# Performance work log

Measured on AMD Instinct MI355X. Metric: run time of the kernel, lower is better.

## Reference

```python
import jax, jax.numpy as jnp
import numpy as np

DIM = 1024
N_HEADS = 16
HEAD_DIM = 64
SEQ = 2048
BATCH = 2


def setup_inputs() -> dict:
    key = jax.random.key(0)
    ks = jax.random.split(key, 7)
    scale = 1.0 / np.sqrt(DIM)
    return {
        "q": jax.random.normal(ks[0], (BATCH, SEQ, DIM), dtype=jnp.float32),
        "k": jax.random.normal(ks[1], (BATCH, SEQ, DIM), dtype=jnp.float32),
        "v": jax.random.normal(ks[2], (BATCH, SEQ, DIM), dtype=jnp.float32),
        "wq": jax.random.normal(ks[3], (DIM, DIM), dtype=jnp.float32) * scale,
        "wk": jax.random.normal(ks[4], (DIM, DIM), dtype=jnp.float32) * scale,
        "wv": jax.random.normal(ks[5], (DIM, DIM), dtype=jnp.float32) * scale,
        "wo": jax.random.normal(ks[6], (DIM, DIM), dtype=jnp.float32) * scale,
    }


def reference(q, k, v, wq, wk, wv, wo):
    B, S, D = q.shape
    # Linear layers: y = x @ W.T (torch nn.Linear convention)
    qh = (q @ wq.T).reshape(B, S, N_HEADS, HEAD_DIM).transpose(0, 2, 1, 3)  # [B,H,S,hd]
    kh = (k @ wk.T).reshape(B, S, N_HEADS, HEAD_DIM).transpose(0, 2, 1, 3)
    vh = (v @ wv.T).reshape(B, S, N_HEADS, HEAD_DIM).transpose(0, 2, 1, 3)
    score = jnp.einsum('bhqd,bhkd->bhqk', qh, kh) / jnp.sqrt(jnp.float32(HEAD_DIM))
    # causal mask: upper triangle (j > i) set to -inf
    causal = jnp.tril(jnp.ones((S, S), dtype=bool))
    score = jnp.where(causal[None, None], score, -jnp.inf)
    attn = jax.nn.softmax(score, axis=-1)
    out = jnp.einsum('bhqk,bhkd->bhqd', attn, vh)  # [B,H,S,hd]
    out = out.transpose(0, 2, 1, 3).reshape(B, S, D)
    return out @ wo.T
```

## Files before the change

kernel.cpp:

```cpp
#include <hip/hip_runtime.h>

typedef unsigned short u16;
typedef unsigned int   u32;
typedef __bf16 bf16x8 __attribute__((ext_vector_type(8)));
typedef float  f32x4  __attribute__((ext_vector_type(4)));
typedef unsigned short u16x4 __attribute__((ext_vector_type(4)));
typedef unsigned short u16x8 __attribute__((ext_vector_type(8)));
typedef unsigned int   u32x2 __attribute__((ext_vector_type(2)));
typedef unsigned int   u32x4 __attribute__((ext_vector_type(4)));

#define DIM   1024
#define SEQ   2048
#define NH    16
#define HD    64
#define NBATCH 2

#define NEG_INF (-__builtin_inff())
#define QSCALE 0.1803368801111204f


__device__ __forceinline__ u16 f2bf(float f) {
  unsigned u = __float_as_uint(f);
  unsigned r = (u + 0x7FFFu + ((u >> 16) & 1u)) >> 16;
  return (u16)r;
}

__device__ __forceinline__ u32 pkbf(float a, float b) {
#if __has_builtin(__builtin_amdgcn_cvt_pk_bf16_f32)
  typedef __bf16 bf16x2 __attribute__((ext_vector_type(2)));
  bf16x2 t = __builtin_amdgcn_cvt_pk_bf16_f32(a, b);
  return __builtin_bit_cast(u32, t);
#else
  return (u32)f2bf(a) | ((u32)f2bf(b) << 16);
#endif
}

__device__ __forceinline__ void gload16(const void* g, void* lds_uniform) {
  __builtin_amdgcn_global_load_lds(
      (__attribute__((address_space(1))) void*)(size_t)g,
      (__attribute__((address_space(3))) void*)lds_uniform,
      16, 0, 0);
}


__global__ __launch_bounds__(256) void cvt_all(
    const float* __restrict__ q, const float* __restrict__ k, const float* __restrict__ v,
    const float* __restrict__ wq, const float* __restrict__ wk, const float* __restrict__ wv,
    const float* __restrict__ wo, u16* __restrict__ ws) {
  const size_t M = 1u << 20;
  int b = blockIdx.x;
  const float* src;
  u16* dst;
  int idx;
  if (b < 6144) {
    int t = b >> 11; idx = b & 2047;
    src = (t == 0) ? q : (t == 1) ? k : v;
    dst = ws + (size_t)t * 4 * M;
  } else {
    int t = (b - 6144) >> 9; idx = (b - 6144) & 511;
    src = (t == 0) ? wq : (t == 1) ? wk : (t == 2) ? wv : wo;
    dst = ws + (12 + (size_t)t) * M;
  }
  size_t i = ((size_t)idx * 256 + threadIdx.x) * 8;
  float4 a = *(const float4*)(src + i);
  float4 c = *(const float4*)(src + i + 4);
  u16x8 o;
  o[0] = f2bf(a.x); o[1] = f2bf(a.y); o[2] = f2bf(a.z); o[3] = f2bf(a.w);
  o[4] = f2bf(c.x); o[5] = f2bf(c.y); o[6] = f2bf(c.z); o[7] = f2bf(c.w);
  *(u16x8*)(dst + i) = o;
}


__device__ __forceinline__ void gemm128_core(const u16* __restrict__ A,
                                             const u16* __restrict__ W,
                                             int bm, int bn,
                                             u16* lds, f32x4 (&acc)[4][4]) {
  const int K = 1024;
  const int tid = threadIdx.x;
  const int wave = tid >> 6, lane = tid & 63;
  const int quad = lane >> 4, l15 = lane & 15;
  const int warp_m = wave >> 1, warp_n = wave & 1;

  const int c0 = wave * 128 + lane, c1 = c0 + 64;
  const u16* Ag0 = A + (size_t)(bm * 128 + (c0 >> 2)) * K + (c0 & 3) * 8;
  const u16* Ag1 = A + (size_t)(bm * 128 + (c1 >> 2)) * K + (c1 & 3) * 8;
  const u16* Wg0 = W + (size_t)(bn * 128 + (c0 >> 2)) * K + (c0 & 3) * 8;
  const u16* Wg1 = W + (size_t)(bn * 128 + (c1 >> 2)) * K + (c1 & 3) * 8;
  const int lA0 = (wave * 2 + 0) * 512;
  const int lA1 = (wave * 2 + 1) * 512;
  const int lB0 = 4096 + (wave * 2 + 0) * 512;
  const int lB1 = 4096 + (wave * 2 + 1) * 512;

  gload16(Ag0, lds + lA0);
  gload16(Ag1, lds + lA1);
  gload16(Wg0, lds + lB0);
  gload16(Wg1, lds + lB1);

  for (int k0 = 0; k0 < K; k0 += 32) {
    const int buf = (k0 >> 5) & 1;
    u16* cur = lds + buf * 8192;
    __syncthreads();
    if (k0 + 32 < K) {
      u16* nxt = lds + (buf ^ 1) * 8192;
      gload16(Ag0 + k0 + 32, nxt + lA0);
      gload16(Ag1 + k0 + 32, nxt + lA1);
      gload16(Wg0 + k0 + 32, nxt + lB0);
      gload16(Wg1 + k0 + 32, nxt + lB1);
    }

    bf16x8 af[4], bfr[4];
#pragma unroll
    for (int i = 0; i < 4; ++i) {
      af[i]  = *(const bf16x8*)(cur + (warp_m * 64 + i * 16 + l15) * 32 + quad * 8);
      bfr[i] = *(const bf16x8*)(cur + 4096 + (warp_n * 64 + i * 16 + l15) * 32 + quad * 8);
    }
#pragma unroll
    for (int i = 0; i < 4; ++i)
#pragma unroll
      for (int j = 0; j < 4; ++j)
        acc[i][j] = __builtin_amdgcn_mfma_f32_16x16x32_bf16(af[i], bfr[j], acc[i][j], 0, 0, 0);
  }
}

__global__ __launch_bounds__(256) void gemm_qkv(
    const u16* __restrict__ qb, const u16* __restrict__ kb, const u16* __restrict__ vb,
    const u16* __restrict__ wq, const u16* __restrict__ wk, const u16* __restrict__ wv,
    u16* __restrict__ Qo, u16* __restrict__ Ko, u16* __restrict__ Vt) {
  __shared__ __align__(16) u16 lds[2][8192];
  const int id = blockIdx.x;
  const int c = id & 7, bn = (id >> 3) & 7, t = id >> 6;
  const int g = c + 8 * t;
  const int bm = g & 31, z = g >> 5;

  const u16* A = (z == 0) ? qb : (z == 1) ? kb : vb;
  const u16* W = (z == 0) ? wq : (z == 1) ? wk : wv;
  f32x4 acc[4][4] = {};
  gemm128_core(A, W, bm, bn, &lds[0][0], acc);

  const int tid = threadIdx.x;
  const int wave = tid >> 6, lane = tid & 63;
  const int quad = lane >> 4, l15 = lane & 15;
  const int warp_m = wave >> 1, warp_n = wave & 1;
#pragma unroll
  for (int i = 0; i < 4; ++i)
#pragma unroll
    for (int j = 0; j < 4; ++j) {
      int s0 = bm * 128 + warp_m * 64 + i * 16 + quad * 4;
      int n  = bn * 128 + warp_n * 64 + j * 16 + l15;
      int bb = s0 >> 11, sl0 = s0 & 2047, h = n >> 6, d = n & 63;
      if (z == 2) {
        int pos = (sl0 & ~63) | (sl0 & 32) | ((sl0 & 12) << 1) | ((sl0 & 16) >> 2);
        int psw = (pos & ~63) | ((((pos >> 3) & 7) ^ (d & 7)) << 3) | (pos & 7);
        u16x4 pv;
        pv[0] = f2bf(acc[i][j][0]); pv[1] = f2bf(acc[i][j][1]);
        pv[2] = f2bf(acc[i][j][2]); pv[3] = f2bf(acc[i][j][3]);
        *(u16x4*)(Vt + ((size_t)(bb * NH + h) * HD + d) * SEQ + psw) = pv;
      } else if (z == 1) {
#pragma unroll
        for (int r = 0; r < 4; ++r) {
          int s = sl0 + r;
          int dsw = (((d >> 3) ^ (s & 7)) << 3) | (d & 7);
          Ko[((size_t)(bb * NH + h) * SEQ + s) * HD + dsw] = f2bf(acc[i][j][r]);
        }
      } else {
#pragma unroll
        for (int r = 0; r < 4; ++r)
          Qo[((size_t)(bb * NH + h) * SEQ + sl0 + r) * HD + d] = f2bf(acc[i][j][r] * QSCALE);
      }
    }
}

__global__ __launch_bounds__(256) void gemm_out(
    const u16* __restrict__ A, const u16* __restrict__ W, float* __restrict__ Out) {
  __shared__ __align__(16) u16 lds[2][8192];
  const int id = blockIdx.x;
  const int bn = (id >> 3) & 7;
  const int bm = (id & 7) + 8 * (id >> 6);
  f32x4 acc[4][4] = {};
  gemm128_core(A, W, bm, bn, &lds[0][0], acc);

  const int tid = threadIdx.x;
  const int wave = tid >> 6, lane = tid & 63;
  const int quad = lane >> 4, l15 = lane & 15;
  const int warp_m = wave >> 1, warp_n = wave & 1;
#pragma unroll
  for (int i = 0; i < 4; ++i)
#pragma unroll
    for (int j = 0; j < 4; ++j)
#pragma unroll
      for (int r = 0; r < 4; ++r) {
        int m = bm * 128 + warp_m * 64 + i * 16 + quad * 4 + r;
        int n = bn * 128 + warp_n * 64 + j * 16 + l15;
        Out[(size_t)m * DIM + n] = acc[i][j][r];
      }
}


__global__ __launch_bounds__(256) void attn_kernel(
    const u16* __restrict__ Q, const u16* __restrict__ K,
    const u16* __restrict__ Vt, u16* __restrict__ O) {
  __shared__ __align__(16) u16 Kl[2][4096];
  __shared__ __align__(16) u16 Vl[2][4096];

  const int tid = threadIdx.x;
  const int wave = tid >> 6, lane = tid & 63;
  const int quad = lane >> 4, l15 = lane & 15;
  const int bx = blockIdx.x;
  const int bh = bx & 31;
  const int qt = 31 - (bx >> 5);
  const int b = bh >> 4, h = bh & 15;

  const u16* qbase = Q + ((size_t)bh * SEQ + qt * 64 + wave * 16 + l15) * HD + quad * 8;
  const bf16x8 qf0 = *(const bf16x8*)(qbase);
  const bf16x8 qf1 = *(const bf16x8*)(qbase + 32);

  bf16x8 ones;
#pragma unroll
  for (int i = 0; i < 8; ++i) ones[i] = (__bf16)1.0f;

  f32x4 o[4] = {};
  f32x4 o4 = {};
  float m_run = NEG_INF;

  const int c0 = wave * 128 + lane, c1 = c0 + 64;
  const u16* Ksrc = K + (size_t)bh * SEQ * HD;
  const u16* Vsrc = Vt + (size_t)bh * HD * SEQ;
  const int sw0 = ((quad ^ (l15 & 7)) << 3);
  const int sw1 = (((4 + quad) ^ (l15 & 7)) << 3);

  {
    gload16(Ksrc + (size_t)c0 * 8, &Kl[0][(wave * 2 + 0) * 512]);
    gload16(Ksrc + (size_t)c1 * 8, &Kl[0][(wave * 2 + 1) * 512]);
    gload16(Vsrc + (size_t)(c0 >> 3) * SEQ + (c0 & 7) * 8, &Vl[0][(wave * 2 + 0) * 512]);
    gload16(Vsrc + (size_t)(c1 >> 3) * SEQ + (c1 & 7) * 8, &Vl[0][(wave * 2 + 1) * 512]);
  }

  for (int kt = 0; kt <= qt; ++kt) {
    const int buf = kt & 1;
    __syncthreads();
    if (kt < qt) {
      const int nb = buf ^ 1;
      const size_t kb = (size_t)(kt + 1) * 64;
      gload16(Ksrc + (kb * HD) + (size_t)c0 * 8, &Kl[nb][(wave * 2 + 0) * 512]);
      gload16(Ksrc + (kb * HD) + (size_t)c1 * 8, &Kl[nb][(wave * 2 + 1) * 512]);
      gload16(Vsrc + (size_t)(c0 >> 3) * SEQ + kb + (c0 & 7) * 8, &Vl[nb][(wave * 2 + 0) * 512]);
      gload16(Vsrc + (size_t)(c1 >> 3) * SEQ + kb + (c1 & 7) * 8, &Vl[nb][(wave * 2 + 1) * 512]);
    }

    f32x4 s[4];
#pragma unroll
    for (int kn = 0; kn < 4; ++kn) {
      const u16* arow = &Kl[buf][(kn * 16 + l15) * 64];
      bf16x8 kf0 = *(const bf16x8*)(arow + sw0);
      bf16x8 kf1 = *(const bf16x8*)(arow + sw1);
      f32x4 z = {};
      z = __builtin_amdgcn_mfma_f32_16x16x32_bf16(kf0, qf0, z, 0, 0, 0);
      z = __builtin_amdgcn_mfma_f32_16x16x32_bf16(kf1, qf1, z, 0, 0, 0);
      s[kn] = z;
    }

    if (kt == qt) {
      const int qloc = wave * 16 + l15;
#pragma unroll
      for (int kn = 0; kn < 4; ++kn)
#pragma unroll
        for (int r = 0; r < 4; ++r)
          if (kn * 16 + quad * 4 + r > qloc) s[kn][r] = NEG_INF;
    }

    float mr = NEG_INF;
#pragma unroll
    for (int kn = 0; kn < 4; ++kn)
#pragma unroll
      for (int r = 0; r < 4; ++r) mr = fmaxf(mr, s[kn][r]);
    mr = fmaxf(mr, __shfl_xor(mr, 16));
    mr = fmaxf(mr, __shfl_xor(mr, 32));
    const float mnew = fmaxf(m_run, mr);
    const float alpha = __builtin_amdgcn_exp2f(m_run - mnew);
    m_run = mnew;
#pragma unroll
    for (int kn = 0; kn < 4; ++kn)
#pragma unroll
      for (int r = 0; r < 4; ++r)
        s[kn][r] = __builtin_amdgcn_exp2f(s[kn][r] - mnew);

    u32x4 t0, t1;
    t0[0] = pkbf(s[0][0], s[0][1]); t0[1] = pkbf(s[0][2], s[0][3]);
    t0[2] = pkbf(s[1][0], s[1][1]); t0[3] = pkbf(s[1][2], s[1][3]);
    t1[0] = pkbf(s[2][0], s[2][1]); t1[1] = pkbf(s[2][2], s[2][3]);
    t1[2] = pkbf(s[3][0], s[3][1]); t1[3] = pkbf(s[3][2], s[3][3]);
    bf16x8 pf0 = __builtin_bit_cast(bf16x8, t0);
    bf16x8 pf1 = __builtin_bit_cast(bf16x8, t1);

#pragma unroll
    for (int n = 0; n < 4; ++n)
#pragma unroll
      for (int r = 0; r < 4; ++r) o[n][r] *= alpha;
#pragma unroll
    for (int r = 0; r < 4; ++r) o4[r] *= alpha;

    o4 = __builtin_amdgcn_mfma_f32_16x16x32_bf16(ones, pf0, o4, 0, 0, 0);
    o4 = __builtin_amdgcn_mfma_f32_16x16x32_bf16(ones, pf1, o4, 0, 0, 0);

#pragma unroll
    for (int n = 0; n < 4; ++n) {
      const u16* vrow = &Vl[buf][(n * 16 + l15) * 64];
      bf16x8 vf0 = *(const bf16x8*)(vrow + sw0);
      bf16x8 vf1 = *(const bf16x8*)(vrow + sw1);
      o[n] = __builtin_amdgcn_mfma_f32_16x16x32_bf16(vf0, pf0, o[n], 0, 0, 0);
      o[n] = __builtin_amdgcn_mfma_f32_16x16x32_bf16(vf1, pf1, o[n], 0, 0, 0);
    }
  }

  const float inv = 1.f / o4[0];
  const int srow = qt * 64 + wave * 16 + l15;
  u16* obase = O + ((size_t)b * SEQ + srow) * DIM + h * HD + quad * 4;
#pragma unroll
  for (int n = 0; n < 4; ++n) {
    u32x2 st;
    st[0] = pkbf(o[n][0] * inv, o[n][1] * inv);
    st[1] = pkbf(o[n][2] * inv, o[n][3] * inv);
    *(u32x2*)(obase + n * 16) = st;
  }
}


extern "C" void kernel_launch(void* const* d_in, const int* in_sizes, int n_in,
                              void* d_out, int out_size, void* d_ws, size_t ws_size,
                              hipStream_t stream) {
  (void)in_sizes; (void)n_in; (void)out_size; (void)ws_size;
  const float* q  = (const float*)d_in[0];
  const float* k  = (const float*)d_in[1];
  const float* v  = (const float*)d_in[2];
  const float* wq = (const float*)d_in[3];
  const float* wk = (const float*)d_in[4];
  const float* wv = (const float*)d_in[5];
  const float* wo = (const float*)d_in[6];

  u16* ws = (u16*)d_ws;
  const size_t EL = 1u << 20;
  u16* QB = ws + 0 * EL;
  u16* KB = ws + 4 * EL;
  u16* VB = ws + 8 * EL;
  u16* WQ = ws + 12 * EL;
  u16* WK = ws + 13 * EL;
  u16* WV = ws + 14 * EL;
  u16* WO = ws + 15 * EL;
  u16* Qw = ws + 16 * EL;
  u16* Kw = ws + 20 * EL;
  u16* Vtw = ws + 24 * EL;
  u16* AO = ws + 28 * EL;

  cvt_all<<<8192, 256, 0, stream>>>(q, k, v, wq, wk, wv, wo, ws);
  gemm_qkv<<<768, 256, 0, stream>>>(QB, KB, VB, WQ, WK, WV, Qw, Kw, Vtw);
  attn_kernel<<<1024, 256, 0, stream>>>(Qw, Kw, Vtw, AO);
  gemm_out<<<256, 256, 0, stream>>>(AO, WO, (float*)d_out);
}
```

Measured before the change: 200.6 us.

## Shrink GEMM tiles to 128x64, swizzle LDS, reorder attention query tiles

Both GEMM kernels switch from 128x128 to 128x64 output tiles, which doubles the grid sizes (768 to 1536 and 256 to 512) to give better occupancy on the many-CU device. The change adds a launch-bounds occupancy hint of 6 blocks for gemm_qkv. It also adds an XOR swizzle on the LDS layout of the K-chunks to cut bank conflicts. The attention kernel's query-tile order becomes a serpentine pattern to balance causal work across waves of blocks. Smaller tiles reduce data reuse per block and add more A-matrix reloads.

```diff
diff --git a/kernel.cpp b/kernel.cpp
--- a/kernel.cpp
+++ b/kernel.cpp
@@ -71,82 +71,76 @@
 }
 
 
-__device__ __forceinline__ void gemm128_core(const u16* __restrict__ A,
-                                             const u16* __restrict__ W,
-                                             int bm, int bn,
-                                             u16* lds, f32x4 (&acc)[4][4]) {
+__global__ __launch_bounds__(256, 6) void gemm_qkv(
+    const u16* __restrict__ qb, const u16* __restrict__ kb, const u16* __restrict__ vb,
+    const u16* __restrict__ wq, const u16* __restrict__ wk, const u16* __restrict__ wv,
+    u16* __restrict__ Qo, u16* __restrict__ Ko, u16* __restrict__ Vt) {
+  __shared__ __align__(16) u16 lds[2][6144];
   const int K = 1024;
+  const int id = blockIdx.x;
+  const int c = id & 7, t = id >> 3;
+  const int z = t >> 6;
+  const int u = t & 63;
+  const int bm = (u >> 4) * 8 + c;
+  const int bn = u & 15;
+
+  const u16* A = (z == 0) ? qb : (z == 1) ? kb : vb;
+  const u16* W = (z == 0) ? wq : (z == 1) ? wk : wv;
+
   const int tid = threadIdx.x;
   const int wave = tid >> 6, lane = tid & 63;
   const int quad = lane >> 4, l15 = lane & 15;
   const int warp_m = wave >> 1, warp_n = wave & 1;
 
   const int c0 = wave * 128 + lane, c1 = c0 + 64;
-  const u16* Ag0 = A + (size_t)(bm * 128 + (c0 >> 2)) * K + (c0 & 3) * 8;
-  const u16* Ag1 = A + (size_t)(bm * 128 + (c1 >> 2)) * K + (c1 & 3) * 8;
-  const u16* Wg0 = W + (size_t)(bn * 128 + (c0 >> 2)) * K + (c0 & 3) * 8;
-  const u16* Wg1 = W + (size_t)(bn * 128 + (c1 >> 2)) * K + (c1 & 3) * 8;
+  const u16* Ag0 = A + (size_t)(bm * 128 + (c0 >> 2)) * K + (((c0 & 3) ^ ((c0 >> 3) & 3)) * 8);
+  const u16* Ag1 = A + (size_t)(bm * 128 + (c1 >> 2)) * K + (((c1 & 3) ^ ((c1 >> 3) & 3)) * 8);
+  const int cw = wave * 64 + lane;
+  const u16* Wg = W + (size_t)(bn * 64 + (cw >> 2)) * K + (((cw & 3) ^ ((cw >> 3) & 3)) * 8);
   const int lA0 = (wave * 2 + 0) * 512;
   const int lA1 = (wave * 2 + 1) * 512;
-  const int lB0 = 4096 + (wave * 2 + 0) * 512;
-  const int lB1 = 4096 + (wave * 2 + 1) * 512;
-
-  gload16(Ag0, lds + lA0);
-  gload16(Ag1, lds + lA1);
-  gload16(Wg0, lds + lB0);
-  gload16(Wg1, lds + lB1);
-
+  const int lB  = 4096 + wave * 512;
+
+  u16* lds0 = &lds[0][0];
+  gload16(Ag0, lds0 + lA0);
+  gload16(Ag1, lds0 + lA1);
+  gload16(Wg,  lds0 + lB);
+
+  f32x4 acc[4][2] = {};
   for (int k0 = 0; k0 < K; k0 += 32) {
     const int buf = (k0 >> 5) & 1;
-    u16* cur = lds + buf * 8192;
+    u16* cur = lds0 + buf * 6144;
     __syncthreads();
     if (k0 + 32 < K) {
-      u16* nxt = lds + (buf ^ 1) * 8192;
+      u16* nxt = lds0 + (buf ^ 1) * 6144;
       gload16(Ag0 + k0 + 32, nxt + lA0);
       gload16(Ag1 + k0 + 32, nxt + lA1);
-      gload16(Wg0 + k0 + 32, nxt + lB0);
-      gload16(Wg1 + k0 + 32, nxt + lB1);
-    }
-
-    bf16x8 af[4], bfr[4];
+      gload16(Wg  + k0 + 32, nxt + lB);
+    }
+    bf16x8 af[4], bfr[2];
 #pragma unroll
     for (int i = 0; i < 4; ++i) {
-      af[i]  = *(const bf16x8*)(cur + (warp_m * 64 + i * 16 + l15) * 32 + quad * 8);
-      bfr[i] = *(const bf16x8*)(cur + 4096 + (warp_n * 64 + i * 16 + l15) * 32 + quad * 8);
+      int ra = warp_m * 64 + i * 16 + l15;
+      af[i] = *(const bf16x8*)(cur + ra * 32 + ((quad ^ ((ra >> 1) & 3)) << 3));
+    }
+#pragma unroll
+    for (int j = 0; j < 2; ++j) {
+      int rb = warp_n * 32 + j * 16 + l15;
+      bfr[j] = *(const bf16x8*)(cur + 4096 + rb * 32 + ((quad ^ ((rb >> 1) & 3)) << 3));
     }
 #pragma unroll
     for (int i = 0; i < 4; ++i)
 #pragma unroll
-      for (int j = 0; j < 4; ++j)
+      for (int j = 0; j < 2; ++j)
         acc[i][j] = __builtin_amdgcn_mfma_f32_16x16x32_bf16(af[i], bfr[j], acc[i][j], 0, 0, 0);
   }
-}
-
-__global__ __launch_bounds__(256) void gemm_qkv(
-    const u16* __restrict__ qb, const u16* __restrict__ kb, const u16* __restrict__ vb,
-    const u16* __restrict__ wq, const u16* __restrict__ wk, const u16* __restrict__ wv,
-    u16* __restrict__ Qo, u16* __restrict__ Ko, u16* __restrict__ Vt) {
-  __shared__ __align__(16) u16 lds[2][8192];
-  const int id = blockIdx.x;
-  const int c = id & 7, bn = (id >> 3) & 7, t = id >> 6;
-  const int g = c + 8 * t;
-  const int bm = g & 31, z = g >> 5;
-
-  const u16* A = (z == 0) ? qb : (z == 1) ? kb : vb;
-  const u16* W = (z == 0) ? wq : (z == 1) ? wk : wv;
-  f32x4 acc[4][4] = {};
-  gemm128_core(A, W, bm, bn, &lds[0][0], acc);
-
-  const int tid = threadIdx.x;
-  const int wave = tid >> 6, lane = tid & 63;
-  const int quad = lane >> 4, l15 = lane & 15;
-  const int warp_m = wave >> 1, warp_n = wave & 1;
+
 #pragma unroll
   for (int i = 0; i < 4; ++i)
 #pragma unroll
-    for (int j = 0; j < 4; ++j) {
+    for (int j = 0; j < 2; ++j) {
       int s0 = bm * 128 + warp_m * 64 + i * 16 + quad * 4;
-      int n  = bn * 128 + warp_n * 64 + j * 16 + l15;
+      int n  = bn * 64 + warp_n * 32 + j * 16 + l15;
       int bb = s0 >> 11, sl0 = s0 & 2047, h = n >> 6, d = n & 63;
       if (z == 2) {
         int pos = (sl0 & ~63) | (sl0 & 32) | ((sl0 & 12) << 1) | ((sl0 & 16) >> 2);
@@ -172,25 +166,67 @@
 
 __global__ __launch_bounds__(256) void gemm_out(
     const u16* __restrict__ A, const u16* __restrict__ W, float* __restrict__ Out) {
-  __shared__ __align__(16) u16 lds[2][8192];
+  __shared__ __align__(16) u16 lds[2][6144];
+  const int K = 1024;
   const int id = blockIdx.x;
-  const int bn = (id >> 3) & 7;
-  const int bm = (id & 7) + 8 * (id >> 6);
-  f32x4 acc[4][4] = {};
-  gemm128_core(A, W, bm, bn, &lds[0][0], acc);
-
+  const int bn = (id >> 3) & 15;
+  const int bm = (id & 7) + 8 * (id >> 7);
   const int tid = threadIdx.x;
   const int wave = tid >> 6, lane = tid & 63;
   const int quad = lane >> 4, l15 = lane & 15;
   const int warp_m = wave >> 1, warp_n = wave & 1;
+
+  const int c0 = wave * 128 + lane, c1 = c0 + 64;
+  const u16* Ag0 = A + (size_t)(bm * 128 + (c0 >> 2)) * K + (((c0 & 3) ^ ((c0 >> 3) & 3)) * 8);
+  const u16* Ag1 = A + (size_t)(bm * 128 + (c1 >> 2)) * K + (((c1 & 3) ^ ((c1 >> 3) & 3)) * 8);
+  const int cw = wave * 64 + lane;
+  const u16* Wg = W + (size_t)(bn * 64 + (cw >> 2)) * K + (((cw & 3) ^ ((cw >> 3) & 3)) * 8);
+  const int lA0 = (wave * 2 + 0) * 512;
+  const int lA1 = (wave * 2 + 1) * 512;
+  const int lB  = 4096 + wave * 512;
+
+  u16* lds0 = &lds[0][0];
+  gload16(Ag0, lds0 + lA0);
+  gload16(Ag1, lds0 + lA1);
+  gload16(Wg,  lds0 + lB);
+
+  f32x4 acc[4][2] = {};
+  for (int k0 = 0; k0 < K; k0 += 32) {
+    const int buf = (k0 >> 5) & 1;
+    u16* cur = lds0 + buf * 6144;
+    __syncthreads();
+    if (k0 + 32 < K) {
+      u16* nxt = lds0 + (buf ^ 1) * 6144;
+      gload16(Ag0 + k0 + 32, nxt + lA0);
+      gload16(Ag1 + k0 + 32, nxt + lA1);
+      gload16(Wg  + k0 + 32, nxt + lB);
+    }
+    bf16x8 af[4], bfr[2];
+#pragma unroll
+    for (int i = 0; i < 4; ++i) {
+      int ra = warp_m * 64 + i * 16 + l15;
+      af[i] = *(const bf16x8*)(cur + ra * 32 + ((quad ^ ((ra >> 1) & 3)) << 3));
+    }
+#pragma unroll
+    for (int j = 0; j < 2; ++j) {
+      int rb = warp_n * 32 + j * 16 + l15;
+      bfr[j] = *(const bf16x8*)(cur + 4096 + rb * 32 + ((quad ^ ((rb >> 1) & 3)) << 3));
+    }
+#pragma unroll
+    for (int i = 0; i < 4; ++i)
+#pragma unroll
+      for (int j = 0; j < 2; ++j)
+        acc[i][j] = __builtin_amdgcn_mfma_f32_16x16x32_bf16(af[i], bfr[j], acc[i][j], 0, 0, 0);
+  }
+
 #pragma unroll
   for (int i = 0; i < 4; ++i)
 #pragma unroll
-    for (int j = 0; j < 4; ++j)
+    for (int j = 0; j < 2; ++j)
 #pragma unroll
       for (int r = 0; r < 4; ++r) {
         int m = bm * 128 + warp_m * 64 + i * 16 + quad * 4 + r;
-        int n = bn * 128 + warp_n * 64 + j * 16 + l15;
+        int n = bn * 64 + warp_n * 32 + j * 16 + l15;
         Out[(size_t)m * DIM + n] = acc[i][j][r];
       }
 }
@@ -207,7 +243,8 @@
   const int quad = lane >> 4, l15 = lane & 15;
   const int bx = blockIdx.x;
   const int bh = bx & 31;
-  const int qt = 31 - (bx >> 5);
+  const int j = bx >> 5, jhi = j >> 3, jlo = j & 7;
+  const int qt = 31 - (jhi * 8 + ((jhi & 1) ? (7 - jlo) : jlo));
   const int b = bh >> 4, h = bh & 15;
 
   const u16* qbase = Q + ((size_t)bh * SEQ + qt * 64 + wave * 16 + l15) * HD + quad * 8;
@@ -352,7 +389,7 @@
   u16* AO = ws + 28 * EL;
 
   cvt_all<<<8192, 256, 0, stream>>>(q, k, v, wq, wk, wv, wo, ws);
-  gemm_qkv<<<768, 256, 0, stream>>>(QB, KB, VB, WQ, WK, WV, Qw, Kw, Vtw);
+  gemm_qkv<<<1536, 256, 0, stream>>>(QB, KB, VB, WQ, WK, WV, Qw, Kw, Vtw);
   attn_kernel<<<1024, 256, 0, stream>>>(Qw, Kw, Vtw, AO);
-  gemm_out<<<256, 256, 0, stream>>>(AO, WO, (float*)d_out);
-}
+  gemm_out<<<512, 256, 0, stream>>>(AO, WO, (float*)d_out);
+}
```

Measured after the change: 207.0 us. +3.2%, slower.
